# Optimization experiments

Measured on AMD Instinct MI355X. Metric: run time of the kernel, lower is better.

Reference implementation:

```python
import jax, jax.numpy as jnp
import numpy as np

H = 8
D = 512
DK = D // H
B = 16
N = 8192


def setup_inputs() -> dict:
    key = jax.random.key(0)
    k1, k2, k3, k4 = jax.random.split(key, 4)
    x = jax.random.normal(k1, (B, N, D), dtype=jnp.float32)
    W_k = jax.random.normal(k2, (D, D), dtype=jnp.float32) * (1.0 / np.sqrt(D))
    W_g = jax.random.normal(k3, (D, D), dtype=jnp.float32) * (1.0 / np.sqrt(D))
    query = jax.random.normal(k4, (H, 1, DK), dtype=jnp.float32)
    return {"x": x, "W_k": W_k, "W_g": W_g, "query": query}


def reference(x, W_k, W_g, query):
    b, n, d = x.shape
    # nn.Linear: y = x @ W.T  (no bias)
    K = (x @ W_k.T).reshape(b, n, H, DK).transpose(0, 2, 1, 3)  # (b,h,n,dk)
    G = (x @ W_g.T).reshape(b, n, H, DK).transpose(0, 2, 1, 3)  # (b,h,n,dk)
    xh = x.reshape(b, n, H, DK).transpose(0, 2, 1, 3)           # (b,h,n,dk)
    gated = jnp.tanh(K) * jax.nn.sigmoid(G)                     # (b,h,n,dk)
    # single-query attention: scores (b,h,1,n)
    scores = jnp.einsum('hmd,bhnd->bhmn', query, gated)
    attn = jax.nn.softmax(scores, axis=-1)
    out = jnp.einsum('bhmn,bhnd->bhmd', attn, xh)               # (b,h,1,dk)
    out = out.transpose(0, 2, 1, 3).reshape(b, 1, H * DK)
    return out.squeeze()  # (b, d)
```

## Files before the change

### kernel.cpp

```cpp
#include <hip/hip_runtime.h>
#include <hip/hip_bf16.h>

#define H_ 8
#define D_ 512
#define DK_ 64
#define B_ 16
#define N_ 8192
#define M_ (B_ * N_)

typedef __attribute__((ext_vector_type(8))) short short8;
typedef __attribute__((ext_vector_type(4))) float floatx4;

__device__ __forceinline__ void glds16(const void* g, void* l) {
    __builtin_amdgcn_global_load_lds((const __attribute__((address_space(1))) void*)g,
                                     (__attribute__((address_space(3))) void*)l,
                                     16, 0, 0);
}

__device__ __forceinline__ unsigned short f2bf(float f) {
    unsigned u = __float_as_uint(f);
    return (unsigned short)((u + 0x7fffu + ((u >> 16) & 1u)) >> 16);
}

__device__ __forceinline__ unsigned pack_bf2(float x, float y) {
    return __builtin_amdgcn_perm(__float_as_uint(y) + 0x8000u,
                                 __float_as_uint(x) + 0x8000u, 0x07060302u);
}

__device__ __forceinline__ short8 pack_bf8(float4 lo, float4 hi) {
    union { unsigned u[4]; short8 s; } tmp;
    tmp.u[0] = pack_bf2(lo.x, lo.y);
    tmp.u[1] = pack_bf2(lo.z, lo.w);
    tmp.u[2] = pack_bf2(hi.x, hi.y);
    tmp.u[3] = pack_bf2(hi.z, hi.w);
    return tmp.s;
}

__global__ __launch_bounds__(256) void cvt_kernel(const float* __restrict__ src,
                                                  unsigned short* __restrict__ dst, int n4) {
    int i = blockIdx.x * blockDim.x + threadIdx.x;
    int stride = gridDim.x * blockDim.x;
    for (; i < n4; i += stride) {
        float4 v = ((const float4*)src)[i];
        ushort4 o;
        o.x = f2bf(v.x); o.y = f2bf(v.y); o.z = f2bf(v.z); o.w = f2bf(v.w);
        ((ushort4*)dst)[i] = o;
    }
}

__global__ __launch_bounds__(256, 2) void gemm_score_kernel(
    const float* __restrict__ x,
    const unsigned short* __restrict__ wkb,
    const unsigned short* __restrict__ wgb,
    const float* __restrict__ query,
    float* __restrict__ s_buf)
{
    __shared__ unsigned short lds_a[128 * 64];
    __shared__ unsigned short lds_k[128 * 64];
    __shared__ unsigned short lds_g[128 * 64];

    const int t = threadIdx.x;
    const int lane = t & 63;
    const int wave = t >> 6;
    const int wm = wave >> 1, wn = wave & 1;

    const int g = blockIdx.x;
    const int xcd = g & 7;
    const int s = g >> 3;
    const int jt = s & 3;
    const int mt = ((s >> 2) << 3) | xcd;
    const int jc = jt * 128;
    const int m0 = mt * 128;

    floatx4 acc_k[4][4], acc_g[4][4];
#pragma unroll
    for (int i = 0; i < 4; ++i)
#pragma unroll
        for (int j = 0; j < 4; ++j) { acc_k[i][j] = (floatx4)0.f; acc_g[i][j] = (floatx4)0.f; }

    const int r0 = t >> 2;
    const int c0 = t & 3;
    const int swr = ((r0 & 1) << 2) ^ ((r0 >> 1) & 3);
    const float* pA0 = x + (size_t)(m0 + r0) * 512 + c0 * 8;
    const float* pA1 = pA0 + 64 * 512;
    unsigned short* wA00 = lds_a + ((r0 * 8) + (c0 ^ swr)) * 8;
    unsigned short* wA01 = lds_a + ((r0 * 8) + ((c0 ^ swr) ^ 4)) * 8;
    unsigned short* wA10 = wA00 + 64 * 64;
    unsigned short* wA11 = wA01 + 64 * 64;

    int boff[4];
#pragma unroll
    for (int i = 0; i < 4; ++i) {
        int p = i * 256 + t;
        int r = p >> 3;
        int c = (p & 7) ^ (((r & 1) << 2) ^ ((r >> 1) & 3));
        boff[i] = (jc + r) * 512 + c * 8;
    }

    const int fr = lane & 15;
    const int q  = lane >> 4;
    const int swf = ((fr & 1) << 2) ^ ((fr >> 1) & 3);

    for (int k0 = 0; k0 < 512; k0 += 64) {
#pragma unroll
        for (int i = 0; i < 4; ++i) {
            glds16(wkb + boff[i] + k0, lds_k + (size_t)(i * 256 + t) * 8);
            glds16(wgb + boff[i] + k0, lds_g + (size_t)(i * 256 + t) * 8);
        }
        float4 a00 = *(const float4*)(pA0 + k0);
        float4 a01 = *(const float4*)(pA0 + k0 + 4);
        float4 a02 = *(const float4*)(pA0 + k0 + 32);
        float4 a03 = *(const float4*)(pA0 + k0 + 36);
        float4 a10 = *(const float4*)(pA1 + k0);
        float4 a11 = *(const float4*)(pA1 + k0 + 4);
        float4 a12 = *(const float4*)(pA1 + k0 + 32);
        float4 a13 = *(const float4*)(pA1 + k0 + 36);
        *(short8*)wA00 = pack_bf8(a00, a01);
        *(short8*)wA01 = pack_bf8(a02, a03);
        *(short8*)wA10 = pack_bf8(a10, a11);
        *(short8*)wA11 = pack_bf8(a12, a13);
        __syncthreads();

#pragma unroll
        for (int kc = 0; kc < 2; ++kc) {
            const int sl = ((kc * 4 + q) ^ swf) * 8;
            short8 a[4], bk[4], bg[4];
#pragma unroll
            for (int mi = 0; mi < 4; ++mi)
                a[mi] = *(const short8*)(lds_a + (wm * 64 + mi * 16 + fr) * 64 + sl);
#pragma unroll
            for (int ni = 0; ni < 4; ++ni) {
                bk[ni] = *(const short8*)(lds_k + (wn * 64 + ni * 16 + fr) * 64 + sl);
                bg[ni] = *(const short8*)(lds_g + (wn * 64 + ni * 16 + fr) * 64 + sl);
            }
#pragma unroll
            for (int mi = 0; mi < 4; ++mi)
#pragma unroll
                for (int ni = 0; ni < 4; ++ni) {
                    acc_k[mi][ni] = __builtin_amdgcn_mfma_f32_16x16x32_bf16(a[mi], bk[ni], acc_k[mi][ni], 0, 0, 0);
                    acc_g[mi][ni] = __builtin_amdgcn_mfma_f32_16x16x32_bf16(a[mi], bg[ni], acc_g[mi][ni], 0, 0, 0);
                }
        }
        __syncthreads();
    }

    const int h = jt * 2 + wn;
    float qv[4];
#pragma unroll
    for (int ni = 0; ni < 4; ++ni) qv[ni] = query[h * 64 + ni * 16 + fr];

#pragma unroll
    for (int mi = 0; mi < 4; ++mi) {
#pragma unroll
        for (int r = 0; r < 4; ++r) {
            float v = 0.f;
#pragma unroll
            for (int ni = 0; ni < 4; ++ni) {
                float kv = acc_k[mi][ni][r];
                float gv = acc_g[mi][ni][r];
                float e2k = __expf(2.f * kv);
                float th = 1.f - 2.f / (e2k + 1.f);
                float sg = 1.f / (1.f + __expf(-gv));
                v += qv[ni] * th * sg;
            }
            v += __shfl_xor(v, 1);
            v += __shfl_xor(v, 2);
            v += __shfl_xor(v, 4);
            v += __shfl_xor(v, 8);
            if (fr == 0) {
                int mg = m0 + wm * 64 + mi * 16 + (lane >> 4) * 4 + r;
                int b = mg >> 13, n = mg & 8191;
                s_buf[((size_t)(b * 8 + h) << 13) + n] = v;
            }
        }
    }
}

__global__ __launch_bounds__(256) void stats_kernel(const float* __restrict__ s_buf,
                                                    float* __restrict__ mb, float* __restrict__ lb) {
    const int bh = blockIdx.x;
    const float* s = s_buf + ((size_t)bh << 13);
    const int t = threadIdx.x;
    float mx = -3.0e38f;
    for (int i = t; i < 8192; i += 256) mx = fmaxf(mx, s[i]);
#pragma unroll
    for (int m = 32; m > 0; m >>= 1) mx = fmaxf(mx, __shfl_xor(mx, m));
    __shared__ float red[8];
    if ((t & 63) == 0) red[t >> 6] = mx;
    __syncthreads();
    mx = fmaxf(fmaxf(red[0], red[1]), fmaxf(red[2], red[3]));
    float sum = 0.f;
    for (int i = t; i < 8192; i += 256) sum += __expf(s[i] - mx);
#pragma unroll
    for (int m = 32; m > 0; m >>= 1) sum += __shfl_xor(sum, m);
    if ((t & 63) == 0) red[4 + (t >> 6)] = sum;
    __syncthreads();
    if (t == 0) { mb[bh] = mx; lb[bh] = red[4] + red[5] + red[6] + red[7]; }
}

__global__ __launch_bounds__(256) void out_kernel(
    const float* __restrict__ x, const float* __restrict__ s_buf,
    const float* __restrict__ mb, const float* __restrict__ lb,
    float* __restrict__ out) {
    const int b = blockIdx.x >> 5;
    const int chunk = blockIdx.x & 31;
    const int n0 = chunk * 256;
    const int t = threadIdx.x;
    __shared__ float w[8 * 256];
    for (int i = t; i < 2048; i += 256) {
        int hh = i >> 8, nn = i & 255;
        int bh = b * 8 + hh;
        w[i] = __expf(s_buf[((size_t)bh << 13) + n0 + nn] - mb[bh]) / lb[bh];
    }
    __syncthreads();
    const int rg = t >> 6;
    const int d0 = (t & 63) * 8;
    const float* wh = w + ((d0 >> 6) << 8);
    float acc[8] = {0.f, 0.f, 0.f, 0.f, 0.f, 0.f, 0.f, 0.f};
    for (int nn = rg; nn < 256; nn += 4) {
        const float4* row = (const float4*)(x + (((size_t)(b * 8192 + n0 + nn)) << 9) + d0);
        float4 v0 = row[0];
        float4 v1 = row[1];
        float ww = wh[nn];
        acc[0] += ww * v0.x; acc[1] += ww * v0.y;
        acc[2] += ww * v0.z; acc[3] += ww * v0.w;
        acc[4] += ww * v1.x; acc[5] += ww * v1.y;
        acc[6] += ww * v1.z; acc[7] += ww * v1.w;
    }
#pragma unroll
    for (int j = 0; j < 8; ++j) atomicAdd(&out[b * 512 + d0 + j], acc[j]);
}

extern "C" void kernel_launch(void* const* d_in, const int* in_sizes, int n_in,
                              void* d_out, int out_size, void* d_ws, size_t ws_size,
                              hipStream_t stream) {
    const float* x  = (const float*)d_in[0];
    const float* Wk = (const float*)d_in[1];
    const float* Wg = (const float*)d_in[2];
    const float* q  = (const float*)d_in[3];
    float* out = (float*)d_out;

    char* ws = (char*)d_ws;
    unsigned short* wkb = (unsigned short*)ws;
    unsigned short* wgb = (unsigned short*)(ws + 524288ull);
    float* s_buf = (float*)(ws + 1048576ull);
    float* mb = (float*)(ws + 5242880ull);
    float* lb = (float*)(ws + 5243392ull);

    hipMemsetAsync(d_out, 0, 512 * B_ * sizeof(float), stream);

    hipLaunchKernelGGL(cvt_kernel, dim3(256), dim3(256), 0, stream, Wk, wkb, (D_ * D_) / 4);
    hipLaunchKernelGGL(cvt_kernel, dim3(256), dim3(256), 0, stream, Wg, wgb, (D_ * D_) / 4);
    hipLaunchKernelGGL(gemm_score_kernel, dim3(4096), dim3(256), 0, stream, x, wkb, wgb, q, s_buf);
    hipLaunchKernelGGL(stats_kernel, dim3(128), dim3(256), 0, stream, s_buf, mb, lb);
    hipLaunchKernelGGL(out_kernel, dim3(512), dim3(256), 0, stream, x, s_buf, mb, lb, out);
}
```

Measured before the change: 585.0 us.

## Double-buffer GEMM with 256-row tiles, 512 threads, and prefetch of next K-slice

Restructures the fused projection-score GEMM to 512-thread blocks covering 256 rows, with double-buffered LDS for both the x tile and the combined Wk/Wg tile. The next K-slice is prefetched (global-to-LDS for weights, registers for x) while MFMAs run on the current buffer, with s_setprio and split barriers. Each head's score is now partially reduced per wave and combined through LDS before the store. It also vectorises the stats kernel with float4 register caching and halves the out_kernel chunk size to launch more blocks. In exchange it uses much more LDS per block and more register pressure, which may limit occupancy.

```diff
diff --git a/kernel.cpp b/kernel.cpp
--- a/kernel.cpp
+++ b/kernel.cpp
@@ -48,21 +48,24 @@
     }
 }
 
-__global__ __launch_bounds__(256, 2) void gemm_score_kernel(
+__global__ __launch_bounds__(512, 2) void gemm_score_kernel(
     const float* __restrict__ x,
     const unsigned short* __restrict__ wkb,
     const unsigned short* __restrict__ wgb,
     const float* __restrict__ query,
     float* __restrict__ s_buf)
 {
-    __shared__ unsigned short lds_a[128 * 64];
-    __shared__ unsigned short lds_k[128 * 64];
-    __shared__ unsigned short lds_g[128 * 64];
+    __shared__ __attribute__((aligned(16))) unsigned short lds_a[2][256 * 64];
+    __shared__ __attribute__((aligned(16))) unsigned short lds_b[2][256 * 64];
 
     const int t = threadIdx.x;
     const int lane = t & 63;
     const int wave = t >> 6;
-    const int wm = wave >> 1, wn = wave & 1;
+    const int wm = wave >> 2;
+    const int wn = wave & 3;
+    const int fr = lane & 15;
+    const int q4 = lane >> 4;
+    const int sw = fr & 7;
 
     const int g = blockIdx.x;
     const int xcd = g & 7;
@@ -70,92 +73,123 @@
     const int jt = s & 3;
     const int mt = ((s >> 2) << 3) | xcd;
     const int jc = jt * 128;
-    const int m0 = mt * 128;
-
-    floatx4 acc_k[4][4], acc_g[4][4];
-#pragma unroll
-    for (int i = 0; i < 4; ++i)
-#pragma unroll
-        for (int j = 0; j < 4; ++j) { acc_k[i][j] = (floatx4)0.f; acc_g[i][j] = (floatx4)0.f; }
-
-    const int r0 = t >> 2;
-    const int c0 = t & 3;
-    const int swr = ((r0 & 1) << 2) ^ ((r0 >> 1) & 3);
-    const float* pA0 = x + (size_t)(m0 + r0) * 512 + c0 * 8;
-    const float* pA1 = pA0 + 64 * 512;
-    unsigned short* wA00 = lds_a + ((r0 * 8) + (c0 ^ swr)) * 8;
-    unsigned short* wA01 = lds_a + ((r0 * 8) + ((c0 ^ swr) ^ 4)) * 8;
-    unsigned short* wA10 = wA00 + 64 * 64;
-    unsigned short* wA11 = wA01 + 64 * 64;
-
-    int boff[4];
-#pragma unroll
-    for (int i = 0; i < 4; ++i) {
-        int p = i * 256 + t;
-        int r = p >> 3;
-        int c = (p & 7) ^ (((r & 1) << 2) ^ ((r >> 1) & 3));
-        boff[i] = (jc + r) * 512 + c * 8;
-    }
-
-    const int fr = lane & 15;
-    const int q  = lane >> 4;
-    const int swf = ((fr & 1) << 2) ^ ((fr >> 1) & 3);
-
-    for (int k0 = 0; k0 < 512; k0 += 64) {
-#pragma unroll
-        for (int i = 0; i < 4; ++i) {
-            glds16(wkb + boff[i] + k0, lds_k + (size_t)(i * 256 + t) * 8);
-            glds16(wgb + boff[i] + k0, lds_g + (size_t)(i * 256 + t) * 8);
+    const int m0 = mt * 256;
+
+    const int ar = t >> 3;
+    const int ac = t & 7;
+    const float* pA = x + (size_t)(m0 + ar) * 512 + ac * 8;
+    const int asw = ac ^ (ar & 7);
+    const int awoff = ar * 64 + asw * 8;
+
+    const unsigned short* pB[4];
+    pB[0] = wkb + (size_t)(jc + ar) * 512 + asw * 8;
+    pB[1] = wkb + (size_t)(jc + 64 + ar) * 512 + asw * 8;
+    pB[2] = wgb + (size_t)(jc + ar) * 512 + asw * 8;
+    pB[3] = wgb + (size_t)(jc + 64 + ar) * 512 + asw * 8;
+
+    const int aroff  = (wm * 128 + fr) * 64 + (q4 ^ sw) * 8;
+    const int bk_off = (wn * 32 + fr) * 64 + (q4 ^ sw) * 8;
+    const int bg_off = bk_off + 128 * 64;
+
+    floatx4 acc_k[8][2], acc_g[8][2];
+#pragma unroll
+    for (int mi = 0; mi < 8; ++mi)
+#pragma unroll
+        for (int ni = 0; ni < 2; ++ni) { acc_k[mi][ni] = (floatx4)0.f; acc_g[mi][ni] = (floatx4)0.f; }
+
+    float4 av[8];
+
+    {
+#pragma unroll
+        for (int it = 0; it < 4; ++it) {
+            const float* p = pA + (size_t)it * (64 * 512);
+            av[it * 2]     = *(const float4*)(p);
+            av[it * 2 + 1] = *(const float4*)(p + 4);
         }
-        float4 a00 = *(const float4*)(pA0 + k0);
-        float4 a01 = *(const float4*)(pA0 + k0 + 4);
-        float4 a02 = *(const float4*)(pA0 + k0 + 32);
-        float4 a03 = *(const float4*)(pA0 + k0 + 36);
-        float4 a10 = *(const float4*)(pA1 + k0);
-        float4 a11 = *(const float4*)(pA1 + k0 + 4);
-        float4 a12 = *(const float4*)(pA1 + k0 + 32);
-        float4 a13 = *(const float4*)(pA1 + k0 + 36);
-        *(short8*)wA00 = pack_bf8(a00, a01);
-        *(short8*)wA01 = pack_bf8(a02, a03);
-        *(short8*)wA10 = pack_bf8(a10, a11);
-        *(short8*)wA11 = pack_bf8(a12, a13);
-        __syncthreads();
-
-#pragma unroll
-        for (int kc = 0; kc < 2; ++kc) {
-            const int sl = ((kc * 4 + q) ^ swf) * 8;
-            short8 a[4], bk[4], bg[4];
-#pragma unroll
-            for (int mi = 0; mi < 4; ++mi)
-                a[mi] = *(const short8*)(lds_a + (wm * 64 + mi * 16 + fr) * 64 + sl);
-#pragma unroll
-            for (int ni = 0; ni < 4; ++ni) {
-                bk[ni] = *(const short8*)(lds_k + (wn * 64 + ni * 16 + fr) * 64 + sl);
-                bg[ni] = *(const short8*)(lds_g + (wn * 64 + ni * 16 + fr) * 64 + sl);
-            }
-#pragma unroll
-            for (int mi = 0; mi < 4; ++mi)
-#pragma unroll
-                for (int ni = 0; ni < 4; ++ni) {
-                    acc_k[mi][ni] = __builtin_amdgcn_mfma_f32_16x16x32_bf16(a[mi], bk[ni], acc_k[mi][ni], 0, 0, 0);
-                    acc_g[mi][ni] = __builtin_amdgcn_mfma_f32_16x16x32_bf16(a[mi], bg[ni], acc_g[mi][ni], 0, 0, 0);
+#pragma unroll
+        for (int i = 0; i < 4; ++i)
+            glds16(pB[i], &lds_b[0][(i * 512 + wave * 64) * 8]);
+#pragma unroll
+        for (int it = 0; it < 4; ++it)
+            *(short8*)&lds_a[0][it * 4096 + awoff] = pack_bf8(av[it * 2], av[it * 2 + 1]);
+    }
+    __syncthreads();
+
+    for (int kt = 0; kt < 8; ++kt) {
+        const int cur = kt & 1, nxt = cur ^ 1;
+        const unsigned short* la = lds_a[cur];
+        const unsigned short* lb = lds_b[cur];
+        const int k0n = (kt + 1) * 64;
+        short8 bk[2][2], bg[2][2];
+
+#pragma unroll
+        for (int p = 0; p < 4; ++p) {
+            short8 a2[2][2];
+#pragma unroll
+            for (int e = 0; e < 2; ++e) {
+                const int mi = p * 2 + e;
+                a2[e][0] = *(const short8*)&la[mi * 1024 + aroff];
+                a2[e][1] = *(const short8*)&la[(mi * 1024 + aroff) ^ 32];
+            }
+            if (p == 0) {
+#pragma unroll
+                for (int ni = 0; ni < 2; ++ni) {
+                    bk[ni][0] = *(const short8*)&lb[ni * 1024 + bk_off];
+                    bk[ni][1] = *(const short8*)&lb[(ni * 1024 + bk_off) ^ 32];
+                    bg[ni][0] = *(const short8*)&lb[ni * 1024 + bg_off];
+                    bg[ni][1] = *(const short8*)&lb[(ni * 1024 + bg_off) ^ 32];
                 }
+                if (kt < 7) {
+#pragma unroll
+                    for (int it = 0; it < 4; ++it) {
+                        const float* pp = pA + (size_t)it * (64 * 512) + k0n;
+                        av[it * 2]     = *(const float4*)(pp);
+                        av[it * 2 + 1] = *(const float4*)(pp + 4);
+                    }
+#pragma unroll
+                    for (int i = 0; i < 4; ++i)
+                        glds16(pB[i] + k0n, &lds_b[nxt][(i * 512 + wave * 64) * 8]);
+                }
+            }
+            __builtin_amdgcn_s_barrier();
+            __builtin_amdgcn_s_setprio(1);
+#pragma unroll
+            for (int e = 0; e < 2; ++e) {
+                const int mi = p * 2 + e;
+#pragma unroll
+                for (int ni = 0; ni < 2; ++ni) {
+#pragma unroll
+                    for (int kk = 0; kk < 2; ++kk) {
+                        acc_k[mi][ni] = __builtin_amdgcn_mfma_f32_16x16x32_bf16(a2[e][kk], bk[ni][kk], acc_k[mi][ni], 0, 0, 0);
+                        acc_g[mi][ni] = __builtin_amdgcn_mfma_f32_16x16x32_bf16(a2[e][kk], bg[ni][kk], acc_g[mi][ni], 0, 0, 0);
+                    }
+                }
+            }
+            __builtin_amdgcn_s_setprio(0);
+            if (p == 3 && kt < 7) {
+#pragma unroll
+                for (int it = 0; it < 4; ++it)
+                    *(short8*)&lds_a[nxt][it * 4096 + awoff] = pack_bf8(av[it * 2], av[it * 2 + 1]);
+            }
+            if (p < 3) __builtin_amdgcn_s_barrier();
         }
         __syncthreads();
     }
 
-    const int h = jt * 2 + wn;
-    float qv[4];
-#pragma unroll
-    for (int ni = 0; ni < 4; ++ni) qv[ni] = query[h * 64 + ni * 16 + fr];
-
-#pragma unroll
-    for (int mi = 0; mi < 4; ++mi) {
+    float* part = (float*)&lds_a[0][0];
+    const int h = jt * 2 + (wn >> 1);
+    const int dbase = (wn & 1) * 32;
+    float qv[2];
+    qv[0] = query[h * 64 + dbase + fr];
+    qv[1] = query[h * 64 + dbase + 16 + fr];
+
+#pragma unroll
+    for (int mi = 0; mi < 8; ++mi) {
 #pragma unroll
         for (int r = 0; r < 4; ++r) {
             float v = 0.f;
 #pragma unroll
-            for (int ni = 0; ni < 4; ++ni) {
+            for (int ni = 0; ni < 2; ++ni) {
                 float kv = acc_k[mi][ni][r];
                 float gv = acc_g[mi][ni][r];
                 float e2k = __expf(2.f * kv);
@@ -167,22 +201,34 @@
             v += __shfl_xor(v, 2);
             v += __shfl_xor(v, 4);
             v += __shfl_xor(v, 8);
-            if (fr == 0) {
-                int mg = m0 + wm * 64 + mi * 16 + (lane >> 4) * 4 + r;
-                int b = mg >> 13, n = mg & 8191;
-                s_buf[((size_t)(b * 8 + h) << 13) + n] = v;
-            }
+            if (fr == 0)
+                part[wn * 256 + wm * 128 + mi * 16 + q4 * 4 + r] = v;
         }
+    }
+    __syncthreads();
+    {
+        const int hw = t >> 8;
+        const int row = t & 255;
+        float val = part[(hw * 2) * 256 + row] + part[(hw * 2 + 1) * 256 + row];
+        int m = m0 + row;
+        int b = m >> 13, n = m & 8191;
+        s_buf[((size_t)(b * 8 + jt * 2 + hw) << 13) + n] = val;
     }
 }
 
 __global__ __launch_bounds__(256) void stats_kernel(const float* __restrict__ s_buf,
                                                     float* __restrict__ mb, float* __restrict__ lb) {
     const int bh = blockIdx.x;
-    const float* s = s_buf + ((size_t)bh << 13);
+    const float4* s4 = (const float4*)(s_buf + ((size_t)bh << 13));
     const int t = threadIdx.x;
+    float4 vv[8];
     float mx = -3.0e38f;
-    for (int i = t; i < 8192; i += 256) mx = fmaxf(mx, s[i]);
+#pragma unroll
+    for (int i = 0; i < 8; ++i) {
+        float4 v = s4[t + i * 256];
+        vv[i] = v;
+        mx = fmaxf(mx, fmaxf(fmaxf(v.x, v.y), fmaxf(v.z, v.w)));
+    }
 #pragma unroll
     for (int m = 32; m > 0; m >>= 1) mx = fmaxf(mx, __shfl_xor(mx, m));
     __shared__ float red[8];
@@ -190,7 +236,11 @@
     __syncthreads();
     mx = fmaxf(fmaxf(red[0], red[1]), fmaxf(red[2], red[3]));
     float sum = 0.f;
-    for (int i = t; i < 8192; i += 256) sum += __expf(s[i] - mx);
+#pragma unroll
+    for (int i = 0; i < 8; ++i) {
+        float4 v = vv[i];
+        sum += __expf(v.x - mx) + __expf(v.y - mx) + __expf(v.z - mx) + __expf(v.w - mx);
+    }
 #pragma unroll
     for (int m = 32; m > 0; m >>= 1) sum += __shfl_xor(sum, m);
     if ((t & 63) == 0) red[4 + (t >> 6)] = sum;
@@ -202,22 +252,22 @@
     const float* __restrict__ x, const float* __restrict__ s_buf,
     const float* __restrict__ mb, const float* __restrict__ lb,
     float* __restrict__ out) {
-    const int b = blockIdx.x >> 5;
-    const int chunk = blockIdx.x & 31;
-    const int n0 = chunk * 256;
+    const int b = blockIdx.x >> 6;
+    const int chunk = blockIdx.x & 63;
+    const int n0 = chunk * 128;
     const int t = threadIdx.x;
-    __shared__ float w[8 * 256];
-    for (int i = t; i < 2048; i += 256) {
-        int hh = i >> 8, nn = i & 255;
+    __shared__ float w[8 * 128];
+    for (int i = t; i < 1024; i += 256) {
+        int hh = i >> 7, nn = i & 127;
         int bh = b * 8 + hh;
         w[i] = __expf(s_buf[((size_t)bh << 13) + n0 + nn] - mb[bh]) / lb[bh];
     }
     __syncthreads();
     const int rg = t >> 6;
     const int d0 = (t & 63) * 8;
-    const float* wh = w + ((d0 >> 6) << 8);
+    const float* wh = w + ((d0 >> 6) << 7);
     float acc[8] = {0.f, 0.f, 0.f, 0.f, 0.f, 0.f, 0.f, 0.f};
-    for (int nn = rg; nn < 256; nn += 4) {
+    for (int nn = rg; nn < 128; nn += 4) {
         const float4* row = (const float4*)(x + (((size_t)(b * 8192 + n0 + nn)) << 9) + d0);
         float4 v0 = row[0];
         float4 v1 = row[1];
@@ -251,7 +301,7 @@
 
     hipLaunchKernelGGL(cvt_kernel, dim3(256), dim3(256), 0, stream, Wk, wkb, (D_ * D_) / 4);
     hipLaunchKernelGGL(cvt_kernel, dim3(256), dim3(256), 0, stream, Wg, wgb, (D_ * D_) / 4);
-    hipLaunchKernelGGL(gemm_score_kernel, dim3(4096), dim3(256), 0, stream, x, wkb, wgb, q, s_buf);
+    hipLaunchKernelGGL(gemm_score_kernel, dim3(2048), dim3(512), 0, stream, x, wkb, wgb, q, s_buf);
     hipLaunchKernelGGL(stats_kernel, dim3(128), dim3(256), 0, stream, s_buf, mb, lb);
-    hipLaunchKernelGGL(out_kernel, dim3(512), dim3(256), 0, stream, x, s_buf, mb, lb, out);
-}
+    hipLaunchKernelGGL(out_kernel, dim3(1024), dim3(256), 0, stream, x, s_buf, mb, lb, out);
+}
```

After: 678.3 us. 15.9% more time.
